# Kernel tuning notes

Hardware: AMD Instinct MI355X
Metric: run time of the kernel (lower is better)

## Reference

```python
import jax, jax.numpy as jnp
import numpy as np
import math

D = 256        # input_size == d_k == d_v (per the module: d_k = input_size)
H = 4          # n_heads
MAX_LEN = 800  # PositionalEncoding max_len
NEG = float(-(2**32) + 1)
LN_EPS = 1e-5


def _make_pe():
    pe = np.zeros((MAX_LEN, D), dtype=np.float32)
    pos = np.arange(MAX_LEN, dtype=np.float32)[:, None]
    div = np.exp(np.arange(0, D, 2, dtype=np.float32) * -(math.log(10000.0) / D))
    pe[:, 0::2] = np.sin(pos * div)
    pe[:, 1::2] = np.cos(pos * div)
    return jnp.asarray(pe)


def setup_inputs() -> dict:
    key = jax.random.key(0)
    ks = jax.random.split(key, 12)
    B, L = 32, 512

    def xavier(k, shape):
        fan_in, fan_out = shape[0], shape[1]
        std = math.sqrt(2.0 / (fan_in + fan_out))
        return jax.random.normal(k, shape, dtype=jnp.float32) * std

    return {
        "Q": jax.random.normal(ks[0], (B, L, D), dtype=jnp.float32),
        "K": jax.random.normal(ks[1], (B, L, D), dtype=jnp.float32),
        "V": jax.random.normal(ks[2], (B, L, D), dtype=jnp.float32),
        "mask": jax.random.randint(ks[3], (B, L), 0, 2).astype(jnp.bool_),
        "pe": _make_pe(),
        "W_q": xavier(ks[4], (D, H * D)),
        "W_k": xavier(ks[5], (D, H * D)),
        "W_v": xavier(ks[6], (D, H * D)),
        "W_o": xavier(ks[7], (H * D, D)),
        "w1": xavier(ks[8], (D, D)),
        "b1": jnp.zeros((D,), dtype=jnp.float32),
        "w2": xavier(ks[9], (D, D)),
        "b2": jnp.zeros((D,), dtype=jnp.float32),
        "gamma": jnp.ones((D,), dtype=jnp.float32),
        "beta": jnp.zeros((D,), dtype=jnp.float32),
    }


def _layer_norm(x, gamma, beta):
    mu = jnp.mean(x, axis=-1, keepdims=True)
    var = jnp.mean(jnp.square(x - mu), axis=-1, keepdims=True)
    return (x - mu) * jax.lax.rsqrt(var + LN_EPS) * gamma + beta


def _mha(Q, K, V, mask, W_q, W_k, W_v, W_o):
    B, Lq, _ = Q.shape
    Lk = K.shape[1]

    def split_heads(X, W, L):
        # (B, L, D) @ (D, H*D) -> (B*H, L, D)
        return (X @ W).reshape(B, L, H, D).transpose(0, 2, 1, 3).reshape(B * H, L, D)

    Qh = split_heads(Q, W_q, Lq)
    Kh = split_heads(K, W_k, Lk)
    Vh = split_heads(V, W_v, Lk)

    scale = D ** 0.5 + 1e-6
    scores = jnp.einsum('bqd,bkd->bqk', Qh, Kh) / scale  # (B*H, Lq, Lk)

    pad = jnp.broadcast_to(mask[:, None, :], (B, H, Lq)).reshape(B * H, Lq)
    pad_mask = jnp.broadcast_to(pad[:, :, None], (B * H, Lq, Lk))
    causal = jnp.triu(jnp.ones((Lq, Lk), dtype=jnp.bool_), k=1)
    full_mask = causal[None] | pad_mask
    scores = jnp.where(full_mask, NEG, scores)

    att = jax.nn.softmax(scores, axis=-1)
    Vatt = jnp.einsum('bqk,bkd->bqd', att, Vh)  # (B*H, Lq, D)
    Vatt = Vatt.reshape(B, H, Lq, D).transpose(0, 2, 1, 3).reshape(B, Lq, H * D)
    return Vatt @ W_o


def reference(Q, K, V, mask, pe, W_q, W_k, W_v, W_o, w1, b1, w2, b2, gamma, beta):
    Lq, Lk, Lv = Q.shape[1], K.shape[1], V.shape[1]
    Qp = Q + pe[None, :Lq]
    Kp = K + pe[None, :Lk]
    Vp = V + pe[None, :Lv]

    Vatt = _mha(Qp, Kp, Vp, mask, W_q, W_k, W_v, W_o)
    X = _layer_norm(Qp + Vatt, gamma, beta)
    ffn = jax.nn.relu(X @ w1.T + b1) @ w2.T + b2
    return _layer_norm(ffn + X, gamma, beta)
```

## Files before the change

kernel.cpp:

```cpp
#include <hip/hip_runtime.h>
#include <stdint.h>

#define SEQ   512
#define DM    256
#define NB    32
#define NH    4
#define HD    (NH * DM)
#define PE_MASK (SEQ * DM - 1)
#define NEGV  (-4294967295.0f)

typedef __attribute__((ext_vector_type(8))) short short8;
typedef __attribute__((ext_vector_type(4))) float f32x4;

#if defined(__has_builtin)
#if __has_builtin(__builtin_amdgcn_global_load_lds)
#define HAS_ASYNC 1
#endif
#endif
#ifndef HAS_ASYNC
#define HAS_ASYNC 0
#endif

__device__ __forceinline__ float b2f(unsigned short u) {
    return __uint_as_float(((uint32_t)u) << 16);
}
__device__ __forceinline__ unsigned short f2b(float f) {
    uint32_t u = __float_as_uint(f);
    u += 0x7fffu + ((u >> 16) & 1u);
    return (unsigned short)(u >> 16);
}

__device__ __forceinline__ int swzb(int b) {
    return b ^ (((b >> 7) & 7) << 4);
}

__global__ __launch_bounds__(256) void mask_canon(
    const unsigned char* __restrict__ raw, int* __restrict__ canon)
{
    __shared__ int enc_byte, enc_odd;
    int tid = threadIdx.x;
    if (tid == 0) { enc_byte = 0; enc_odd = 0; }
    __syncthreads();
    if (tid < 255 && raw[tid * 4 + 1]) atomicOr(&enc_byte, 1);
    if (tid < 128 && ((const int*)raw)[tid * 2 + 1]) atomicOr(&enc_odd, 1);
    __syncthreads();
    int i = blockIdx.x * 256 + tid;
    int v;
    if (enc_byte)      v = (raw[i] != 0);
    else if (enc_odd)  v = (((const int*)raw)[i] != 0);
    else               v = ((((const int*)raw)[i * 2] | ((const int*)raw)[i * 2 + 1]) != 0);
    canon[i] = v;
}

__global__ __launch_bounds__(256) void addpe3(
    const float* __restrict__ Q, const float* __restrict__ K,
    const float* __restrict__ V, const float* __restrict__ pe,
    unsigned short* __restrict__ Qp, unsigned short* __restrict__ Kp,
    unsigned short* __restrict__ Vp)
{
    int blk = blockIdx.x;
    int seg = blk >> 12;
    const float* X = (seg == 0) ? Q : (seg == 1) ? K : V;
    unsigned short* O = (seg == 0) ? Qp : (seg == 1) ? Kp : Vp;
    long i = (long)((blk & 4095) * 256 + threadIdx.x) * 4;
    float4 x = *reinterpret_cast<const float4*>(X + i);
    float4 p = *reinterpret_cast<const float4*>(pe + (i & PE_MASK));
    ushort4 o;
    o.x = f2b(x.x + p.x); o.y = f2b(x.y + p.y);
    o.z = f2b(x.z + p.z); o.w = f2b(x.w + p.w);
    *reinterpret_cast<ushort4*>(O + i) = o;
}

__global__ __launch_bounds__(256) void conv2(
    const float* __restrict__ w1, const float* __restrict__ w2,
    unsigned short* __restrict__ o1, unsigned short* __restrict__ o2)
{
    int blk = blockIdx.x;
    const float* in = (blk < 64) ? w1 : w2;
    unsigned short* out = (blk < 64) ? o1 : o2;
    long i = (long)((blk & 63) * 256 + threadIdx.x) * 4;
    float4 x = *reinterpret_cast<const float4*>(in + i);
    ushort4 o;
    o.x = f2b(x.x); o.y = f2b(x.y); o.z = f2b(x.z); o.w = f2b(x.w);
    *reinterpret_cast<ushort4*>(out + i) = o;
}

__global__ __launch_bounds__(256) void transpose_f2b3(
    const float* __restrict__ in0, const float* __restrict__ in1,
    const float* __restrict__ in2, unsigned short* __restrict__ out,
    int ldin, int ldout, long outStride)
{
    int z = blockIdx.z;
    const float* in = (z == 0) ? in0 : (z == 1) ? in1 : in2;
    unsigned short* op = out + z * outStride;
    __shared__ unsigned short tile[32][33];
    int r0 = blockIdx.y * 32, c0 = blockIdx.x * 32;
    int i = threadIdx.x >> 3;
    int j = (threadIdx.x & 7) * 4;
    float4 v = *reinterpret_cast<const float4*>(in + (long)(r0 + i) * ldin + c0 + j);
    tile[i][j + 0] = f2b(v.x); tile[i][j + 1] = f2b(v.y);
    tile[i][j + 2] = f2b(v.z); tile[i][j + 3] = f2b(v.w);
    __syncthreads();
    ushort4 w;
    w.x = tile[j + 0][i]; w.y = tile[j + 1][i]; w.z = tile[j + 2][i]; w.w = tile[j + 3][i];
    *reinterpret_cast<ushort4*>(op + (long)(c0 + i) * ldout + r0 + j) = w;
}

__global__ __launch_bounds__(256) void transpose_f2b(
    const float* __restrict__ in, unsigned short* __restrict__ out,
    int ldin, int ldout)
{
    __shared__ unsigned short tile[32][33];
    int r0 = blockIdx.y * 32, c0 = blockIdx.x * 32;
    int i = threadIdx.x >> 3;
    int j = (threadIdx.x & 7) * 4;
    float4 v = *reinterpret_cast<const float4*>(in + (long)(r0 + i) * ldin + c0 + j);
    tile[i][j + 0] = f2b(v.x); tile[i][j + 1] = f2b(v.y);
    tile[i][j + 2] = f2b(v.z); tile[i][j + 3] = f2b(v.w);
    __syncthreads();
    ushort4 w;
    w.x = tile[j + 0][i]; w.y = tile[j + 1][i]; w.z = tile[j + 2][i]; w.w = tile[j + 3][i];
    *reinterpret_cast<ushort4*>(out + (long)(c0 + i) * ldout + r0 + j) = w;
}

__global__ __launch_bounds__(256) void transpose_bf16(
    const unsigned short* __restrict__ in, unsigned short* __restrict__ out,
    int ldin, int ldout, long sInB, long sInH, long sOutB, long sOutH, int Hdiv)
{
    int z = blockIdx.z; int b = z / Hdiv; int h = z % Hdiv;
    const unsigned short* ip = in + b * sInB + h * sInH;
    unsigned short* op = out + b * sOutB + h * sOutH;
    __shared__ unsigned short tile[32][33];
    int r0 = blockIdx.y * 32, c0 = blockIdx.x * 32;
    int i = threadIdx.x >> 3;
    int j = (threadIdx.x & 7) * 4;
    ushort4 v = *reinterpret_cast<const ushort4*>(ip + (long)(r0 + i) * ldin + c0 + j);
    tile[i][j + 0] = v.x; tile[i][j + 1] = v.y; tile[i][j + 2] = v.z; tile[i][j + 3] = v.w;
    __syncthreads();
    ushort4 w;
    w.x = tile[j + 0][i]; w.y = tile[j + 1][i]; w.z = tile[j + 2][i]; w.w = tile[j + 3][i];
    *reinterpret_cast<ushort4*>(op + (long)(c0 + i) * ldout + r0 + j) = w;
}

__global__ __launch_bounds__(256) void vmean_part(
    const unsigned short* __restrict__ Vh, float* __restrict__ part)
{
    int bl = blockIdx.x, seg = blockIdx.y;
    const unsigned short* p = Vh + (long)bl * SEQ * HD + (long)seg * 64 * HD;
    int c = threadIdx.x * 4;
    float s0 = 0.f, s1 = 0.f, s2 = 0.f, s3 = 0.f;
    for (int l = 0; l < 64; ++l) {
        ushort4 v = *reinterpret_cast<const ushort4*>(p + (long)l * HD + c);
        s0 += b2f(v.x); s1 += b2f(v.y); s2 += b2f(v.z); s3 += b2f(v.w);
    }
    float4 o = {s0, s1, s2, s3};
    *reinterpret_cast<float4*>(part + (long)(bl * 8 + seg) * HD + c) = o;
}

__global__ __launch_bounds__(256) void vmean_reduce(
    const float* __restrict__ part, unsigned short* __restrict__ Vm)
{
    int bl = blockIdx.x;
    int c = threadIdx.x * 4;
    const float* p = part + (long)bl * 8 * HD + c;
    float s0 = 0.f, s1 = 0.f, s2 = 0.f, s3 = 0.f;
#pragma unroll
    for (int seg = 0; seg < 8; ++seg) {
        float4 v = *reinterpret_cast<const float4*>(p + (long)seg * HD);
        s0 += v.x; s1 += v.y; s2 += v.z; s3 += v.w;
    }
    const float inv = 1.0f / SEQ;
    ushort4 o;
    o.x = f2b(s0 * inv); o.y = f2b(s1 * inv);
    o.z = f2b(s2 * inv); o.w = f2b(s3 * inv);
    *reinterpret_cast<ushort4*>(Vm + (long)bl * HD + c) = o;
}

__global__ __launch_bounds__(256) void fix_mask(
    const unsigned short* __restrict__ Vm, unsigned short* __restrict__ Vatt,
    const int* __restrict__ maskc, int b0)
{
    int row = blockIdx.x;
    int bl = row >> 9, l = row & (SEQ - 1);
    if (maskc[(long)(b0 + bl) * SEQ + l] == 0) return;
    int c = threadIdx.x * 4;
    ushort4 v = *reinterpret_cast<const ushort4*>(Vm + (long)bl * HD + c);
    *reinterpret_cast<ushort4*>(Vatt + (long)row * HD + c) = v;
}

template<bool BIAS, bool RELU, bool OUTBF16>
__global__ __launch_bounds__(256) void gemm_bt(
    const unsigned short* __restrict__ A, int lda,
    const unsigned short* __restrict__ B, int ldb,
    void* __restrict__ Cv, int ldc,
    const float* __restrict__ bias, float scale, int K, int Hdiv,
    long sAb, long sAh, long sAz,
    long sBb, long sBh, long sBz,
    long sCb, long sCh, long sCz)
{
    const int m0 = blockIdx.y * 128;
    const int n0 = blockIdx.x * 128;
    int z  = blockIdx.z;
    int bb = z / Hdiv, hh = z % Hdiv;
    const unsigned short* Ab = A + bb * sAb + hh * sAh + (long)z * sAz;
    const unsigned short* Bb = B + bb * sBb + hh * sBh + (long)z * sBz;
    long coff = bb * sCb + hh * sCh + (long)z * sCz;

    __shared__ unsigned short As[128 * 32];
    __shared__ unsigned short Bs[128 * 32];

    const int tid  = threadIdx.x;
    const int lane = tid & 63;
    const int wave = tid >> 6;
    const int wm   = (wave >> 1) * 64;
    const int wn   = (wave & 1) * 64;
    const int lm   = lane & 15;
    const int kq   = (lane >> 4) * 8;

    f32x4 acc[4][4] = {};

    for (int k0 = 0; k0 < K; k0 += 32) {
#pragma unroll
        for (int it = 0; it < 2; ++it) {
            int id = tid + it * 256;
            int r  = id >> 2;
            int c8 = (id & 3) * 8;
            const unsigned short* gA = Ab + (long)(m0 + r) * lda + k0 + c8;
            const unsigned short* gB = Bb + (long)(n0 + r) * ldb + k0 + c8;
#if HAS_ASYNC
            unsigned short* lA = &As[(size_t)(it * 256 + wave * 64) * 8];
            unsigned short* lB = &Bs[(size_t)(it * 256 + wave * 64) * 8];
            __builtin_amdgcn_global_load_lds(
                (const __attribute__((address_space(1))) void*)gA,
                (__attribute__((address_space(3))) void*)lA, 16, 0, 0);
            __builtin_amdgcn_global_load_lds(
                (const __attribute__((address_space(1))) void*)gB,
                (__attribute__((address_space(3))) void*)lB, 16, 0, 0);
#else
            *reinterpret_cast<uint4*>(&As[(size_t)id * 8]) =
                *reinterpret_cast<const uint4*>(gA);
            *reinterpret_cast<uint4*>(&Bs[(size_t)id * 8]) =
                *reinterpret_cast<const uint4*>(gB);
#endif
        }
        __syncthreads();

        short8 af[4], bfr[4];
#pragma unroll
        for (int i = 0; i < 4; ++i)
            af[i] = *reinterpret_cast<const short8*>(&As[(wm + i * 16 + lm) * 32 + kq]);
#pragma unroll
        for (int j = 0; j < 4; ++j)
            bfr[j] = *reinterpret_cast<const short8*>(&Bs[(wn + j * 16 + lm) * 32 + kq]);
#pragma unroll
        for (int i = 0; i < 4; ++i)
#pragma unroll
            for (int j = 0; j < 4; ++j)
                acc[i][j] = __builtin_amdgcn_mfma_f32_16x16x32_bf16(af[i], bfr[j], acc[i][j], 0, 0, 0);
        __syncthreads();
    }

#pragma unroll
    for (int j = 0; j < 4; ++j) {
        int col  = n0 + wn + j * 16 + lm;
        float bv = 0.f;
        if (BIAS) bv = bias[col];
#pragma unroll
        for (int i = 0; i < 4; ++i) {
#pragma unroll
            for (int r = 0; r < 4; ++r) {
                int row = m0 + wm + i * 16 + (lane >> 4) * 4 + r;
                float v = acc[i][j][r] * scale + bv;
                if (RELU) v = fmaxf(v, 0.f);
                long idx = coff + (long)row * ldc + col;
                if (OUTBF16) reinterpret_cast<unsigned short*>(Cv)[idx] = f2b(v);
                else         reinterpret_cast<float*>(Cv)[idx] = v;
            }
        }
    }
}

__device__ __forceinline__ void stage_k32(
    unsigned short* __restrict__ buf, const unsigned short* __restrict__ Ak,
    int kc, int tid, int wave)
{
#pragma unroll
    for (int it = 0; it < 8; ++it) {
        int id = tid + it * 256;
#if HAS_ASYNC
        int U = swzb(id * 16);
        const unsigned short* g = Ak + (long)(U >> 6) * HD + kc * 32 + ((U >> 4) & 3) * 8;
        unsigned short* l = buf + (size_t)(it * 256 + wave * 64) * 8;
        __builtin_amdgcn_global_load_lds(
            (const __attribute__((address_space(1))) void*)g,
            (__attribute__((address_space(3))) void*)l, 16, 0, 0);
#else
        const unsigned short* g = Ak + (long)(id >> 2) * HD + kc * 32 + (id & 3) * 8;
        *reinterpret_cast<uint4*>((char*)buf + swzb(id * 16)) =
            *reinterpret_cast<const uint4*>(g);
#endif
    }
}

__device__ __forceinline__ void stage_v32(
    unsigned short* __restrict__ buf, const unsigned short* __restrict__ Av,
    int chunk, int tid, int wave)
{
#pragma unroll
    for (int it = 0; it < 4; ++it) {
        int id = tid + it * 256;
#if HAS_ASYNC
        int U = swzb(id * 16);
        const unsigned short* g = Av + (long)(U >> 6) * SEQ + chunk * 32 + ((U >> 4) & 3) * 8;
        unsigned short* l = buf + (size_t)(it * 256 + wave * 64) * 8;
        __builtin_amdgcn_global_load_lds(
            (const __attribute__((address_space(1))) void*)g,
            (__attribute__((address_space(3))) void*)l, 16, 0, 0);
#else
        const unsigned short* g = Av + (long)(id >> 2) * SEQ + chunk * 32 + (id & 3) * 8;
        *reinterpret_cast<uint4*>((char*)buf + swzb(id * 16)) =
            *reinterpret_cast<const uint4*>(g);
#endif
    }
}

__global__ __launch_bounds__(256, 2) void flash_attn(
    const unsigned short* __restrict__ Qh,
    const unsigned short* __restrict__ Kh,
    const unsigned short* __restrict__ VhT,
    unsigned short* __restrict__ Vatt,
    const int* __restrict__ maskc, int bh0, float scale, int nbh)
{
    const int tid  = threadIdx.x;
    const int lane = tid & 63;
    const int wave = tid >> 6;
    const int lm   = lane & 15;
    const int qg   = lane >> 4;
    const int kq   = qg * 8;

    const int L = blockIdx.x;
    int z, qt;
    if ((nbh & 7) == 0) {
        int x = L & 7, m = L >> 3;
        qt = m & 7;
        z  = x + 8 * (m >> 3);
    } else {
        z = L % nbh; qt = L / nbh;
    }
    const int b_l = z >> 2, h = z & 3;
    const int m0  = qt * 64;
    const int wq0 = m0 + wave * 16;
    const long qkbase = (long)b_l * SEQ * HD + (long)h * DM;
    const unsigned short* Aq = Qh + qkbase;
    const unsigned short* Ak = Kh + qkbase;
    const unsigned short* Av = VhT + (long)b_l * SEQ * HD + (long)h * SEQ * DM;
    unsigned short* Ov = Vatt + qkbase;
    const int bglob = (bh0 + z) >> 2;

    __shared__ unsigned short Ks[2 * SEQ * 32];
    __shared__ __align__(16) unsigned short Pw[4][16][40];

    f32x4 S[32] = {};
    const int NT = (m0 >> 4) + wave + 1;

    stage_k32(Ks, Ak, 0, tid, wave);
    __syncthreads();
    for (int kc = 0; kc < 8; ++kc) {
        unsigned short* cur = (kc & 1) ? (Ks + SEQ * 32) : Ks;
        unsigned short* nxt = (kc & 1) ? Ks : (Ks + SEQ * 32);
        short8 qf = *reinterpret_cast<const short8*>(
            Aq + (long)(wq0 + lm) * HD + kc * 32 + kq);
        if (kc < 7) {
            stage_k32(nxt, Ak, kc + 1, tid, wave);
        } else {
            stage_v32(Ks, Av, 0, tid, wave);
        }
#pragma unroll
        for (int nt = 0; nt < 32; ++nt) {
            if (nt < NT) {
                int row = nt * 16 + lm;
                short8 bf = *reinterpret_cast<const short8*>(
                    (const char*)cur + swzb(row * 64 + qg * 16));
                S[nt] = __builtin_amdgcn_mfma_f32_16x16x32_bf16(qf, bf, S[nt], 0, 0, 0);
            }
        }
        __syncthreads();
    }

    int   qrow[4];
    bool  rowm[4];
    float mx[4], sm[4];
#pragma unroll
    for (int r = 0; r < 4; ++r) {
        int q = wq0 + qg * 4 + r;
        qrow[r] = q;
        rowm[r] = maskc[bglob * SEQ + q] != 0;
        mx[r] = -3.4e38f;
    }
#pragma unroll
    for (int nt = 0; nt < 32; ++nt) {
        int k = nt * 16 + lm;
#pragma unroll
        for (int r = 0; r < 4; ++r) {
            float v = S[nt][r] * scale;
            if (k > qrow[r]) v = NEGV;
            S[nt][r] = v;
            mx[r] = fmaxf(mx[r], v);
        }
    }
#pragma unroll
    for (int r = 0; r < 4; ++r) {
#pragma unroll
        for (int off = 8; off >= 1; off >>= 1)
            mx[r] = fmaxf(mx[r], __shfl_xor(mx[r], off));
        sm[r] = 0.f;
    }
    uint32_t pk[32][2];
#pragma unroll
    for (int nt = 0; nt < 32; ++nt) {
        float e0 = __expf(S[nt][0] - mx[0]);
        float e1 = __expf(S[nt][1] - mx[1]);
        float e2 = __expf(S[nt][2] - mx[2]);
        float e3 = __expf(S[nt][3] - mx[3]);
        sm[0] += e0; sm[1] += e1; sm[2] += e2; sm[3] += e3;
        pk[nt][0] = (uint32_t)f2b(e0) | ((uint32_t)f2b(e1) << 16);
        pk[nt][1] = (uint32_t)f2b(e2) | ((uint32_t)f2b(e3) << 16);
    }
#pragma unroll
    for (int r = 0; r < 4; ++r) {
#pragma unroll
        for (int off = 8; off >= 1; off >>= 1)
            sm[r] += __shfl_xor(sm[r], off);
        sm[r] = 1.0f / sm[r];
    }

    unsigned short* Vb0 = Ks;
    unsigned short* Vb1 = Ks + 8192;
    const int KC = 2 * (qt + 1);
    f32x4 O[16] = {};
#pragma unroll
    for (int kc2 = 0; kc2 < 16; ++kc2) {
        if (kc2 < KC) {
            unsigned short* Vcur = (kc2 & 1) ? Vb1 : Vb0;
            __syncthreads();
            if (kc2 + 1 < KC) {
                unsigned short* Vnext = (kc2 & 1) ? Vb0 : Vb1;
                stage_v32(Vnext, Av, kc2 + 1, tid, wave);
            }
#pragma unroll
            for (int t = 0; t < 2; ++t) {
                int nt = kc2 * 2 + t;
#pragma unroll
                for (int r = 0; r < 4; ++r)
                    Pw[wave][qg * 4 + r][t * 16 + lm] =
                        (unsigned short)(pk[nt][r >> 1] >> ((r & 1) * 16));
            }
            short8 pf = *reinterpret_cast<const short8*>(&Pw[wave][lm][kq]);
#pragma unroll
            for (int nt2 = 0; nt2 < 16; ++nt2) {
                int row = nt2 * 16 + lm;
                short8 vf = *reinterpret_cast<const short8*>(
                    (const char*)Vcur + swzb(row * 64 + qg * 16));
                O[nt2] = __builtin_amdgcn_mfma_f32_16x16x32_bf16(pf, vf, O[nt2], 0, 0, 0);
            }
        }
    }

#pragma unroll
    for (int nt2 = 0; nt2 < 16; ++nt2) {
#pragma unroll
        for (int r = 0; r < 4; ++r) {
            if (!rowm[r]) {
                int l = wq0 + qg * 4 + r;
                Ov[(long)l * HD + nt2 * 16 + lm] = f2b(O[nt2][r] * sm[r]);
            }
        }
    }
}

__global__ __launch_bounds__(256) void ln1_kernel(
    const unsigned short* __restrict__ AttO, const float* __restrict__ Q,
    const float* __restrict__ pe,
    const float* __restrict__ gamma, const float* __restrict__ beta,
    float* __restrict__ outf, unsigned short* __restrict__ outb)
{
    int row  = blockIdx.x * 4 + (threadIdx.x >> 6);
    int lane = threadIdx.x & 63;
    long base = (long)row * DM + lane * 4;
    ushort4 a = *reinterpret_cast<const ushort4*>(AttO + base);
    float4 qv = *reinterpret_cast<const float4*>(Q + base);
    float4 pv = *reinterpret_cast<const float4*>(pe + (base & PE_MASK));
    float x[4] = {b2f(a.x) + qv.x + pv.x, b2f(a.y) + qv.y + pv.y,
                  b2f(a.z) + qv.z + pv.z, b2f(a.w) + qv.w + pv.w};
    float s = x[0] + x[1] + x[2] + x[3];
#pragma unroll
    for (int off = 32; off > 0; off >>= 1) s += __shfl_xor(s, off);
    float mu = s * (1.0f / DM);
    float vs = 0.f;
#pragma unroll
    for (int t = 0; t < 4; ++t) { float d = x[t] - mu; vs += d * d; }
#pragma unroll
    for (int off = 32; off > 0; off >>= 1) vs += __shfl_xor(vs, off);
    float inv = rsqrtf(vs * (1.0f / DM) + 1e-5f);
    int d0 = lane * 4;
    float4 g = *reinterpret_cast<const float4*>(gamma + d0);
    float4 bt = *reinterpret_cast<const float4*>(beta + d0);
    float4 o;
    o.x = (x[0] - mu) * inv * g.x + bt.x;
    o.y = (x[1] - mu) * inv * g.y + bt.y;
    o.z = (x[2] - mu) * inv * g.z + bt.z;
    o.w = (x[3] - mu) * inv * g.w + bt.w;
    *reinterpret_cast<float4*>(outf + base) = o;
    ushort4 ob;
    ob.x = f2b(o.x); ob.y = f2b(o.y); ob.z = f2b(o.z); ob.w = f2b(o.w);
    *reinterpret_cast<ushort4*>(outb + base) = ob;
}

__global__ __launch_bounds__(256) void ln2_kernel(
    const float* __restrict__ F, const float* __restrict__ X,
    const float* __restrict__ gamma, const float* __restrict__ beta,
    float* __restrict__ out)
{
    int row  = blockIdx.x * 4 + (threadIdx.x >> 6);
    int lane = threadIdx.x & 63;
    long base = (long)row * DM + lane * 4;
    float4 a = *reinterpret_cast<const float4*>(F + base);
    float4 c = *reinterpret_cast<const float4*>(X + base);
    float x[4] = {a.x + c.x, a.y + c.y, a.z + c.z, a.w + c.w};
    float s = x[0] + x[1] + x[2] + x[3];
#pragma unroll
    for (int off = 32; off > 0; off >>= 1) s += __shfl_xor(s, off);
    float mu = s * (1.0f / DM);
    float vs = 0.f;
#pragma unroll
    for (int t = 0; t < 4; ++t) { float d = x[t] - mu; vs += d * d; }
#pragma unroll
    for (int off = 32; off > 0; off >>= 1) vs += __shfl_xor(vs, off);
    float inv = rsqrtf(vs * (1.0f / DM) + 1e-5f);
    int d0 = lane * 4;
    float4 g = *reinterpret_cast<const float4*>(gamma + d0);
    float4 bt = *reinterpret_cast<const float4*>(beta + d0);
    float4 o;
    o.x = (x[0] - mu) * inv * g.x + bt.x;
    o.y = (x[1] - mu) * inv * g.y + bt.y;
    o.z = (x[2] - mu) * inv * g.z + bt.z;
    o.w = (x[3] - mu) * inv * g.w + bt.w;
    *reinterpret_cast<float4*>(out + base) = o;
}

extern "C" void kernel_launch(void* const* d_in, const int* in_sizes, int n_in,
                              void* d_out, int out_size, void* d_ws, size_t ws_size,
                              hipStream_t stream)
{
    const float* Q  = (const float*)d_in[0];
    const float* Ki = (const float*)d_in[1];
    const float* Vi = (const float*)d_in[2];
    const unsigned char* mask_raw = (const unsigned char*)d_in[3];
    const float* pe = (const float*)d_in[4];
    const float* Wq = (const float*)d_in[5];
    const float* Wk = (const float*)d_in[6];
    const float* Wv = (const float*)d_in[7];
    const float* Wo = (const float*)d_in[8];
    const float* w1 = (const float*)d_in[9];
    const float* b1 = (const float*)d_in[10];
    const float* w2 = (const float*)d_in[11];
    const float* b2 = (const float*)d_in[12];
    const float* gamma = (const float*)d_in[13];
    const float* beta  = (const float*)d_in[14];
    float* out = (float*)d_out;

    const size_t MiB = 1048576;
    char* ws = (char*)d_ws;

    int CB = 1;
    for (int cb = 32; cb >= 1; cb >>= 1) {
        size_t scr_sz = (size_t)(5 * cb) * MiB + (size_t)cb * 34816;
        if (scr_sz < 24 * MiB) scr_sz = 24 * MiB;
        if ((59 * MiB + scr_sz) <= ws_size) { CB = cb; break; }
    }
    const int NCH = NB / CB;

    unsigned short* WqT  = (unsigned short*)(ws);
    unsigned short* WkT  = WqT + 262144;
    unsigned short* WvT  = WkT + 262144;
    unsigned short* WoT  = WvT + 262144;
    unsigned short* w1b  = (unsigned short*)(ws + 2 * MiB);
    unsigned short* w2b  = w1b + 65536;
    int*            maskc = (int*)(ws + 2 * MiB + 262144);
    unsigned short* Qp   = (unsigned short*)(ws + 3 * MiB);
    unsigned short* Kp   = (unsigned short*)(ws + 11 * MiB);
    unsigned short* Vp   = (unsigned short*)(ws + 19 * MiB);
    unsigned short* AttO = (unsigned short*)(ws + 27 * MiB);
    unsigned short* Xb   = (unsigned short*)(ws + 35 * MiB);
    float*          Xf   = (float*)(ws + 43 * MiB);
    char*           scr  = ws + 59 * MiB;
    unsigned short* Qh   = (unsigned short*)(scr);
    unsigned short* Kh   = (unsigned short*)(scr + (size_t)CB * MiB);
    unsigned short* Vh   = (unsigned short*)(scr + (size_t)2 * CB * MiB);
    unsigned short* VhT  = (unsigned short*)(scr + (size_t)3 * CB * MiB);
    unsigned short* Vatt = (unsigned short*)(scr + (size_t)4 * CB * MiB);
    float*          part = (float*)(scr + (size_t)5 * CB * MiB);
    unsigned short* Vm   = (unsigned short*)(scr + (size_t)5 * CB * MiB
                                             + (size_t)CB * 8 * HD * 4);
    unsigned short* H1   = (unsigned short*)(scr);
    float*          Ff   = (float*)(scr + 8 * MiB);

    const float scale = (float)(1.0 / (16.0 + 1e-6));
    const long CROWS = (long)CB * SEQ;
    const long CBELT = (long)CB * MiB / 2;

    mask_canon<<<64, 256, 0, stream>>>(mask_raw, maskc);
    transpose_f2b3<<<dim3(32, 8, 3), 256, 0, stream>>>(Wq, Wk, Wv, WqT, HD, DM, 262144);
    transpose_f2b<<<dim3(8, 32, 1), 256, 0, stream>>>(Wo, WoT, DM, HD);
    conv2<<<128, 256, 0, stream>>>(w1, w2, w1b, w2b);
    addpe3<<<12288, 256, 0, stream>>>(Q, Ki, Vi, pe, Qp, Kp, Vp);

    for (int c = 0; c < NCH; ++c) {
        const long r0   = (long)c * CROWS;
        const int  bh0  = c * CB * NH;
        const int  gy   = (int)(CROWS / 128);
        const int  nbh  = CB * NH;

        gemm_bt<false, false, true><<<dim3(8, gy, 3), 256, 0, stream>>>(
            Qp + r0 * DM, DM, WqT, DM, Qh, HD, nullptr, 1.f, DM,
            1, 4194304, 0, 0, 262144, 0, 0, CBELT, 0, 0);

        transpose_bf16<<<dim3(8, 16, CB * NH), 256, 0, stream>>>(
            Vh, VhT, HD, SEQ, (long)SEQ * HD, DM, (long)SEQ * HD, (long)SEQ * DM, NH);

        vmean_part<<<dim3(CB, 8), 256, 0, stream>>>(Vh, part);
        vmean_reduce<<<CB, 256, 0, stream>>>(part, Vm);

        flash_attn<<<dim3(8 * nbh, 1, 1), 256, 0, stream>>>(
            Qh, Kh, VhT, Vatt, maskc, bh0, scale, nbh);

        fix_mask<<<(int)CROWS, 256, 0, stream>>>(Vm, Vatt, maskc, c * CB);

        gemm_bt<false, false, true><<<dim3(2, gy, 1), 256, 0, stream>>>(
            Vatt, HD, WoT, HD, AttO + r0 * DM, DM, nullptr, 1.f, HD,
            1, 0,0,0, 0,0,0, 0,0,0);
    }

    ln1_kernel<<<4096, 256, 0, stream>>>(AttO, Q, pe, gamma, beta, Xf, Xb);

    gemm_bt<true, true, true><<<dim3(2, 128, 1), 256, 0, stream>>>(
        Xb, DM, w1b, DM, H1, DM, b1, 1.f, DM, 1, 0,0,0, 0,0,0, 0,0,0);
    gemm_bt<true, false, false><<<dim3(2, 128, 1), 256, 0, stream>>>(
        H1, DM, w2b, DM, Ff, DM, b2, 1.f, DM, 1, 0,0,0, 0,0,0, 0,0,0);

    ln2_kernel<<<4096, 256, 0, stream>>>(Ff, Xf, gamma, beta, out);
}
```

Before: 348.1 us.

## Fold softmax scale into Q projection, use exp2, widen V chunks, trim K staging

```diff
diff --git a/kernel.cpp b/kernel.cpp
--- a/kernel.cpp
+++ b/kernel.cpp
@@ -28,6 +28,11 @@
     uint32_t u = __float_as_uint(f);
     u += 0x7fffu + ((u >> 16) & 1u);
     return (unsigned short)(u >> 16);
+}
+__device__ __forceinline__ float fast_exp2(float x) {
+    float r;
+    asm("v_exp_f32 %0, %1" : "=v"(r) : "v"(x));
+    return r;
 }
 
 __device__ __forceinline__ int swzb(int b) {
@@ -180,12 +185,14 @@
     const unsigned short* __restrict__ Vm, unsigned short* __restrict__ Vatt,
     const int* __restrict__ maskc, int b0)
 {
-    int row = blockIdx.x;
+    int row = blockIdx.x * 4 + (threadIdx.x >> 6);
     int bl = row >> 9, l = row & (SEQ - 1);
     if (maskc[(long)(b0 + bl) * SEQ + l] == 0) return;
-    int c = threadIdx.x * 4;
-    ushort4 v = *reinterpret_cast<const ushort4*>(Vm + (long)bl * HD + c);
-    *reinterpret_cast<ushort4*>(Vatt + (long)row * HD + c) = v;
+    int c = (threadIdx.x & 63) * 16;
+    uint4 a = *reinterpret_cast<const uint4*>(Vm + (long)bl * HD + c);
+    uint4 b = *reinterpret_cast<const uint4*>(Vm + (long)bl * HD + c + 8);
+    *reinterpret_cast<uint4*>(Vatt + (long)row * HD + c) = a;
+    *reinterpret_cast<uint4*>(Vatt + (long)row * HD + c + 8) = b;
 }
 
 template<bool BIAS, bool RELU, bool OUTBF16>
@@ -205,6 +212,7 @@
     const unsigned short* Ab = A + bb * sAb + hh * sAh + (long)z * sAz;
     const unsigned short* Bb = B + bb * sBb + hh * sBh + (long)z * sBz;
     long coff = bb * sCb + hh * sCh + (long)z * sCz;
+    const float scl = (z == 0) ? scale : 1.0f;
 
     __shared__ unsigned short As[128 * 32];
     __shared__ unsigned short Bs[128 * 32];
@@ -270,7 +278,7 @@
 #pragma unroll
             for (int r = 0; r < 4; ++r) {
                 int row = m0 + wm + i * 16 + (lane >> 4) * 4 + r;
-                float v = acc[i][j][r] * scale + bv;
+                float v = acc[i][j][r] * scl + bv;
                 if (RELU) v = fmaxf(v, 0.f);
                 long idx = coff + (long)row * ldc + col;
                 if (OUTBF16) reinterpret_cast<unsigned short*>(Cv)[idx] = f2b(v);
@@ -282,10 +290,9 @@
 
 __device__ __forceinline__ void stage_k32(
     unsigned short* __restrict__ buf, const unsigned short* __restrict__ Ak,
-    int kc, int tid, int wave)
-{
-#pragma unroll
-    for (int it = 0; it < 8; ++it) {
+    int kc, int qt, int tid, int wave)
+{
+    for (int it = 0; it <= qt; ++it) {
         int id = tid + it * 256;
 #if HAS_ASYNC
         int U = swzb(id * 16);
@@ -302,22 +309,22 @@
     }
 }
 
-__device__ __forceinline__ void stage_v32(
+__device__ __forceinline__ void stage_v64(
     unsigned short* __restrict__ buf, const unsigned short* __restrict__ Av,
-    int chunk, int tid, int wave)
-{
-#pragma unroll
-    for (int it = 0; it < 4; ++it) {
+    int c64, int tid, int wave)
+{
+#pragma unroll
+    for (int it = 0; it < 8; ++it) {
         int id = tid + it * 256;
 #if HAS_ASYNC
         int U = swzb(id * 16);
-        const unsigned short* g = Av + (long)(U >> 6) * SEQ + chunk * 32 + ((U >> 4) & 3) * 8;
+        const unsigned short* g = Av + (long)(U >> 7) * SEQ + c64 * 64 + ((U >> 4) & 7) * 8;
         unsigned short* l = buf + (size_t)(it * 256 + wave * 64) * 8;
         __builtin_amdgcn_global_load_lds(
             (const __attribute__((address_space(1))) void*)g,
             (__attribute__((address_space(3))) void*)l, 16, 0, 0);
 #else
-        const unsigned short* g = Av + (long)(id >> 2) * SEQ + chunk * 32 + (id & 3) * 8;
+        const unsigned short* g = Av + (long)(id >> 3) * SEQ + c64 * 64 + (id & 7) * 8;
         *reinterpret_cast<uint4*>((char*)buf + swzb(id * 16)) =
             *reinterpret_cast<const uint4*>(g);
 #endif
@@ -329,7 +336,7 @@
     const unsigned short* __restrict__ Kh,
     const unsigned short* __restrict__ VhT,
     unsigned short* __restrict__ Vatt,
-    const int* __restrict__ maskc, int bh0, float scale, int nbh)
+    const int* __restrict__ maskc, int bh0, int nbh)
 {
     const int tid  = threadIdx.x;
     const int lane = tid & 63;
@@ -342,7 +349,8 @@
     int z, qt;
     if ((nbh & 7) == 0) {
         int x = L & 7, m = L >> 3;
-        qt = m & 7;
+        int mq = m & 7;
+        qt = (mq & 1) ? (7 - (mq >> 1)) : (mq >> 1);
         z  = x + 8 * (m >> 3);
     } else {
         z = L % nbh; qt = L / nbh;
@@ -363,7 +371,7 @@
     f32x4 S[32] = {};
     const int NT = (m0 >> 4) + wave + 1;
 
-    stage_k32(Ks, Ak, 0, tid, wave);
+    stage_k32(Ks, Ak, 0, qt, tid, wave);
     __syncthreads();
     for (int kc = 0; kc < 8; ++kc) {
         unsigned short* cur = (kc & 1) ? (Ks + SEQ * 32) : Ks;
@@ -371,10 +379,11 @@
         short8 qf = *reinterpret_cast<const short8*>(
             Aq + (long)(wq0 + lm) * HD + kc * 32 + kq);
         if (kc < 7) {
-            stage_k32(nxt, Ak, kc + 1, tid, wave);
+            stage_k32(nxt, Ak, kc + 1, qt, tid, wave);
         } else {
-            stage_v32(Ks, Av, 0, tid, wave);
+            stage_v64(Ks, Av, 0, tid, wave);
         }
+        __builtin_amdgcn_s_setprio(1);
 #pragma unroll
         for (int nt = 0; nt < 32; ++nt) {
             if (nt < NT) {
@@ -384,6 +393,7 @@
                 S[nt] = __builtin_amdgcn_mfma_f32_16x16x32_bf16(qf, bf, S[nt], 0, 0, 0);
             }
         }
+        __builtin_amdgcn_s_setprio(0);
         __syncthreads();
     }
 
@@ -402,7 +412,7 @@
         int k = nt * 16 + lm;
 #pragma unroll
         for (int r = 0; r < 4; ++r) {
-            float v = S[nt][r] * scale;
+            float v = S[nt][r];
             if (k > qrow[r]) v = NEGV;
             S[nt][r] = v;
             mx[r] = fmaxf(mx[r], v);
@@ -418,10 +428,10 @@
     uint32_t pk[32][2];
 #pragma unroll
     for (int nt = 0; nt < 32; ++nt) {
-        float e0 = __expf(S[nt][0] - mx[0]);
-        float e1 = __expf(S[nt][1] - mx[1]);
-        float e2 = __expf(S[nt][2] - mx[2]);
-        float e3 = __expf(S[nt][3] - mx[3]);
+        float e0 = fast_exp2(S[nt][0] - mx[0]);
+        float e1 = fast_exp2(S[nt][1] - mx[1]);
+        float e2 = fast_exp2(S[nt][2] - mx[2]);
+        float e3 = fast_exp2(S[nt][3] - mx[3]);
         sm[0] += e0; sm[1] += e1; sm[2] += e2; sm[3] += e3;
         pk[nt][0] = (uint32_t)f2b(e0) | ((uint32_t)f2b(e1) << 16);
         pk[nt][1] = (uint32_t)f2b(e2) | ((uint32_t)f2b(e3) << 16);
@@ -435,33 +445,38 @@
     }
 
     unsigned short* Vb0 = Ks;
-    unsigned short* Vb1 = Ks + 8192;
-    const int KC = 2 * (qt + 1);
+    unsigned short* Vb1 = Ks + 16384;
+    const int NC = qt + 1;
     f32x4 O[16] = {};
 #pragma unroll
-    for (int kc2 = 0; kc2 < 16; ++kc2) {
-        if (kc2 < KC) {
-            unsigned short* Vcur = (kc2 & 1) ? Vb1 : Vb0;
+    for (int c64 = 0; c64 < 8; ++c64) {
+        if (c64 < NC) {
+            unsigned short* Vcur = (c64 & 1) ? Vb1 : Vb0;
             __syncthreads();
-            if (kc2 + 1 < KC) {
-                unsigned short* Vnext = (kc2 & 1) ? Vb0 : Vb1;
-                stage_v32(Vnext, Av, kc2 + 1, tid, wave);
+            if (c64 + 1 < NC) {
+                unsigned short* Vnext = (c64 & 1) ? Vb0 : Vb1;
+                stage_v64(Vnext, Av, c64 + 1, tid, wave);
             }
 #pragma unroll
             for (int t = 0; t < 2; ++t) {
-                int nt = kc2 * 2 + t;
-#pragma unroll
-                for (int r = 0; r < 4; ++r)
-                    Pw[wave][qg * 4 + r][t * 16 + lm] =
-                        (unsigned short)(pk[nt][r >> 1] >> ((r & 1) * 16));
-            }
-            short8 pf = *reinterpret_cast<const short8*>(&Pw[wave][lm][kq]);
-#pragma unroll
-            for (int nt2 = 0; nt2 < 16; ++nt2) {
-                int row = nt2 * 16 + lm;
-                short8 vf = *reinterpret_cast<const short8*>(
-                    (const char*)Vcur + swzb(row * 64 + qg * 16));
-                O[nt2] = __builtin_amdgcn_mfma_f32_16x16x32_bf16(pf, vf, O[nt2], 0, 0, 0);
+#pragma unroll
+                for (int tt = 0; tt < 2; ++tt) {
+                    int nt = c64 * 4 + t * 2 + tt;
+#pragma unroll
+                    for (int r = 0; r < 4; ++r)
+                        Pw[wave][qg * 4 + r][tt * 16 + lm] =
+                            (unsigned short)(pk[nt][r >> 1] >> ((r & 1) * 16));
+                }
+                short8 pf = *reinterpret_cast<const short8*>(&Pw[wave][lm][kq]);
+                __builtin_amdgcn_s_setprio(1);
+#pragma unroll
+                for (int nt2 = 0; nt2 < 16; ++nt2) {
+                    int row = nt2 * 16 + lm;
+                    short8 vf = *reinterpret_cast<const short8*>(
+                        (const char*)Vcur + swzb(row * 128 + t * 64 + qg * 16));
+                    O[nt2] = __builtin_amdgcn_mfma_f32_16x16x32_bf16(pf, vf, O[nt2], 0, 0, 0);
+                }
+                __builtin_amdgcn_s_setprio(0);
             }
         }
     }
@@ -605,7 +620,7 @@
     unsigned short* H1   = (unsigned short*)(scr);
     float*          Ff   = (float*)(scr + 8 * MiB);
 
-    const float scale = (float)(1.0 / (16.0 + 1e-6));
+    const float SCALE_Q = (float)((1.0 / (16.0 + 1e-6)) * 1.4426950408889634);
     const long CROWS = (long)CB * SEQ;
     const long CBELT = (long)CB * MiB / 2;
 
@@ -622,7 +637,7 @@
         const int  nbh  = CB * NH;
 
         gemm_bt<false, false, true><<<dim3(8, gy, 3), 256, 0, stream>>>(
-            Qp + r0 * DM, DM, WqT, DM, Qh, HD, nullptr, 1.f, DM,
+            Qp + r0 * DM, DM, WqT, DM, Qh, HD, nullptr, SCALE_Q, DM,
             1, 4194304, 0, 0, 262144, 0, 0, CBELT, 0, 0);
 
         transpose_bf16<<<dim3(8, 16, CB * NH), 256, 0, stream>>>(
@@ -632,9 +647,9 @@
         vmean_reduce<<<CB, 256, 0, stream>>>(part, Vm);
 
         flash_attn<<<dim3(8 * nbh, 1, 1), 256, 0, stream>>>(
-            Qh, Kh, VhT, Vatt, maskc, bh0, scale, nbh);
-
-        fix_mask<<<(int)CROWS, 256, 0, stream>>>(Vm, Vatt, maskc, c * CB);
+            Qh, Kh, VhT, Vatt, maskc, bh0, nbh);
+
+        fix_mask<<<(int)(CROWS / 4), 256, 0, stream>>>(Vm, Vatt, maskc, c * CB);
 
         gemm_bt<false, false, true><<<dim3(2, gy, 1), 256, 0, stream>>>(
             Vatt, HD, WoT, HD, AttO + r0 * DM, DM, nullptr, 1.f, HD,
```

After: 345.9 us. Within noise of the previous version (-0.6%).
